# Optimization experiments

Hardware: AMD Instinct MI355X
Metric: run time of the kernel (lower is better)

## Reference

```python
import jax, jax.numpy as jnp
import numpy as np

B, T = 16, 40
NH, DEPTH, NCLASS, IMG_H, W_IMG = 128, 2, 6625, 32, 512
HIDDEN = 64  # nh < 256 -> hidden = 64
LINEAR_IN = NH * 8  # nh * int((32-3-1)/4+1)
BN_EPS = 1e-5


def _conv2d(x, w, b, stride, pad, groups=1):
    y = jax.lax.conv_general_dilated(
        x, w, (stride, stride), [(pad, pad), (pad, pad)],
        dimension_numbers=('NCHW', 'OIHW', 'NCHW'), feature_group_count=groups)
    return y + b[None, :, None, None]


def _conv_bn_act(x, w, b, g, bb, m, v, stride, pad, groups=1):
    y = _conv2d(x, w, b, stride, pad, groups)
    y = (y - m[None, :, None, None]) * jax.lax.rsqrt(v[None, :, None, None] + BN_EPS) \
        * g[None, :, None, None] + bb[None, :, None, None]
    return jax.nn.gelu(y, approximate=False)  # torch nn.GELU default = exact erf


def _gru(xs, wih, whh, bih, bhh):
    # torch GRU gate order: r, z, n. xs: [B, T, D] -> ys: [B, T, H]
    H = whh.shape[1]
    xp = jnp.einsum('btd,gd->btg', xs, wih) + bih  # [B,T,3H]

    def step(h, xt):
        hp = h @ whh.T + bhh
        r = jax.nn.sigmoid(xt[:, :H] + hp[:, :H])
        z = jax.nn.sigmoid(xt[:, H:2 * H] + hp[:, H:2 * H])
        n = jnp.tanh(xt[:, 2 * H:] + r * hp[:, 2 * H:])
        hn = (1.0 - z) * n + z * h
        return hn, hn

    h0 = jnp.zeros((xs.shape[0], H), xs.dtype)
    _, ys = jax.lax.scan(step, h0, jnp.swapaxes(xp, 0, 1))
    return jnp.swapaxes(ys, 0, 1)


def _forward(x, targets,
             conv0_w, conv0_b, bn0_g, bn0_b, bn0_m, bn0_v,
             blk_dw_w, blk_dw_b, blk_bn1_g, blk_bn1_b, blk_bn1_m, blk_bn1_v,
             blk_pw_w, blk_pw_b, blk_bn2_g, blk_bn2_b, blk_bn2_m, blk_bn2_v,
             enc_wih, enc_whh, enc_bih, enc_bhh,
             dec_wih, dec_whh, dec_bih, dec_bhh,
             emb, q_w, q_b, k_w, k_b, e_w, e_b, fc_w, fc_b):
    h = _conv_bn_act(x, conv0_w, conv0_b, bn0_g, bn0_b, bn0_m, bn0_v, 4, 0)  # [B,NH,8,128]
    # NOTE: original code applies each MicroBlock to the SAME x (feat = block(x)); faithful here.
    feat = h
    for i in range(DEPTH):
        t = h + _conv_bn_act(h, blk_dw_w[i], blk_dw_b[i], blk_bn1_g[i], blk_bn1_b[i],
                             blk_bn1_m[i], blk_bn1_v[i], 1, 1, groups=NH)
        feat = _conv_bn_act(t, blk_pw_w[i], blk_pw_b[i], blk_bn2_g[i], blk_bn2_b[i],
                            blk_bn2_m[i], blk_bn2_v[i], 1, 0)
    Bq, C, Hf, Wf = feat.shape
    feat_v = feat.reshape(Bq, C * Hf, Wf)  # Flatten(1,2)
    # adaptive_avg_pool1d target = W/4 == Wf -> identity
    feat_v = jnp.transpose(feat_v, (0, 2, 1))  # [B, Wf, C*Hf]
    enc = _gru(feat_v, enc_wih, enc_whh, enc_bih, enc_bhh)  # [B,Wf,H]
    out_enc = enc[:, -1:, :]  # [B,1,H]
    tgt = emb[targets]  # [B,T,H]
    in_dec = jnp.concatenate([out_enc, tgt], axis=1)  # [B,T+1,H]
    y = _gru(in_dec, dec_wih, dec_whh, dec_bih, dec_bhh)  # [B,T+1,H]
    q = y @ q_w.T + q_b  # [B,Td,NH]
    k = _conv2d(feat, k_w, k_b, 1, 1)  # [B,NH,h,w]
    t2 = jnp.tanh(k[:, None] + q[:, :, :, None, None])  # [B,Td,NH,h,w]
    e = jnp.einsum('btchw,c->bthw', t2, e_w[0]) + e_b[0]  # conv1x1_2: Linear(NH,1)
    a = jax.nn.softmax(e.reshape(Bq, e.shape[1], -1), axis=-1).reshape(e.shape)
    attn_feat = jnp.einsum('bchw,bthw->btc', feat, a)  # [B,Td,NH]
    # dropout: eval mode -> identity
    return attn_feat @ fc_w.T + fc_b  # [B,Td,NCLASS]


def setup_inputs() -> dict:
    key = jax.random.key(0)
    ks = iter(jax.random.split(key, 64))

    def rn(shape, s=0.05):
        return jax.random.normal(next(ks), shape, jnp.float32) * s

    inp = {
        'x': jax.random.normal(next(ks), (B, 3, IMG_H, W_IMG), jnp.float32),
        'targets': jax.random.randint(next(ks), (B, T), 0, NCLASS),
        'conv0_w': rn((NH, 3, 4, 4)), 'conv0_b': rn((NH,)),
        'bn0_g': jnp.ones((NH,)), 'bn0_b': jnp.zeros((NH,)),
        'bn0_m': jnp.zeros((NH,)), 'bn0_v': jnp.ones((NH,)),
        'blk_dw_w': rn((DEPTH, NH, 1, 3, 3)), 'blk_dw_b': rn((DEPTH, NH)),
        'blk_bn1_g': jnp.ones((DEPTH, NH)), 'blk_bn1_b': jnp.zeros((DEPTH, NH)),
        'blk_bn1_m': jnp.zeros((DEPTH, NH)), 'blk_bn1_v': jnp.ones((DEPTH, NH)),
        'blk_pw_w': rn((DEPTH, NH, NH, 1, 1)), 'blk_pw_b': rn((DEPTH, NH)),
        'blk_bn2_g': jnp.ones((DEPTH, NH)), 'blk_bn2_b': jnp.zeros((DEPTH, NH)),
        'blk_bn2_m': jnp.zeros((DEPTH, NH)), 'blk_bn2_v': jnp.ones((DEPTH, NH)),
        'enc_wih': rn((3 * HIDDEN, LINEAR_IN)), 'enc_whh': rn((3 * HIDDEN, HIDDEN)),
        'enc_bih': jnp.zeros((3 * HIDDEN,)), 'enc_bhh': jnp.zeros((3 * HIDDEN,)),
        'dec_wih': rn((3 * HIDDEN, HIDDEN)), 'dec_whh': rn((3 * HIDDEN, HIDDEN)),
        'dec_bih': jnp.zeros((3 * HIDDEN,)), 'dec_bhh': jnp.zeros((3 * HIDDEN,)),
        'emb': rn((NCLASS, HIDDEN)).at[1].set(0.0),  # padding_idx=1
        'q_w': rn((NH, HIDDEN)), 'q_b': jnp.zeros((NH,)),
        'k_w': rn((NH, NH, 3, 3)), 'k_b': jnp.zeros((NH,)),
        'e_w': rn((1, NH)), 'e_b': jnp.zeros((1,)),
        'fc_w': rn((NCLASS, NH)), 'fc_b': jnp.zeros((NCLASS,)),
    }
    return inp


def reference(x, targets,
              conv0_w, conv0_b, bn0_g, bn0_b, bn0_m, bn0_v,
              blk_dw_w, blk_dw_b, blk_bn1_g, blk_bn1_b, blk_bn1_m, blk_bn1_v,
              blk_pw_w, blk_pw_b, blk_bn2_g, blk_bn2_b, blk_bn2_m, blk_bn2_v,
              enc_wih, enc_whh, enc_bih, enc_bhh,
              dec_wih, dec_whh, dec_bih, dec_bhh,
              emb, q_w, q_b, k_w, k_b, e_w, e_b, fc_w, fc_b):
    return _forward(x, targets,
                    conv0_w, conv0_b, bn0_g, bn0_b, bn0_m, bn0_v,
                    blk_dw_w, blk_dw_b, blk_bn1_g, blk_bn1_b, blk_bn1_m, blk_bn1_v,
                    blk_pw_w, blk_pw_b, blk_bn2_g, blk_bn2_b, blk_bn2_m, blk_bn2_v,
                    enc_wih, enc_whh, enc_bih, enc_bhh,
                    dec_wih, dec_whh, dec_bih, dec_bhh,
                    emb, q_w, q_b, k_w, k_b, e_w, e_b, fc_w, fc_b)
```

## Files before the change

### kernel.cpp

```cpp
#include <hip/hip_runtime.h>
#include <hip/hip_bf16.h>

#define DEV __device__ __forceinline__

#define B_    16
#define T_    40
#define TDEC  41
#define NH    128
#define HF    8
#define WF    128
#define HID   64
#define G3    192
#define NCLS  6625
#define SPAT  1024
#define NFRAG 415

typedef _Float16 half8 __attribute__((ext_vector_type(8)));
typedef _Float16 half2_ __attribute__((ext_vector_type(2)));
typedef float    f32x4 __attribute__((ext_vector_type(4)));
typedef float    f32x2 __attribute__((ext_vector_type(2)));

#if __has_builtin(__builtin_amdgcn_fdot2)
#define FDOT2(w,h,acc) __builtin_amdgcn_fdot2((w),(h),(acc),false)
#else
#define FDOT2(w,h,acc) ((acc) + (float)((w)[0])*(float)((h)[0]) + (float)((w)[1])*(float)((h)[1]))
#endif

DEV float sigmoidf_(float x){ return 1.0f/(1.0f + __expf(-x)); }
DEV float tanhf_(float x){ float e = __expf(2.0f*x); return 1.0f - 2.0f/(e + 1.0f); }
DEV float gelu_(float x){ return 0.5f*x*(1.0f + erff(x*0.70710678118654752f)); }
DEV float bnf_(float x, float g, float b, float m, float v){
  return (x - m)*rsqrtf(v + 1e-5f)*g + b;
}

__global__ __launch_bounds__(256) void k_conv0(const float* __restrict__ x,
    const float* __restrict__ w, const float* __restrict__ bias,
    const float* __restrict__ bng, const float* __restrict__ bnb,
    const float* __restrict__ bnm, const float* __restrict__ bnv,
    float* __restrict__ h)
{
  int tid = blockIdx.x*256 + threadIdx.x;
  int ow = tid & 127;
  int oh = (tid >> 7) & 7;
  int c4 = (tid >> 10) & 31;
  int b  = tid >> 15;
  float acc[4] = {0.f,0.f,0.f,0.f};
  int xbase = ((b*3)*32 + oh*4)*512 + ow*4;
  for (int ci = 0; ci < 3; ++ci){
    #pragma unroll
    for (int kh = 0; kh < 4; ++kh){
      float4 xv = *(const float4*)(x + xbase + ci*(32*512) + kh*512);
      #pragma unroll
      for (int cc = 0; cc < 4; ++cc){
        int co = c4*4 + cc;
        const float* wp = w + ((co*3 + ci)*4 + kh)*4;
        acc[cc] += xv.x*wp[0] + xv.y*wp[1] + xv.z*wp[2] + xv.w*wp[3];
      }
    }
  }
  #pragma unroll
  for (int cc = 0; cc < 4; ++cc){
    int co = c4*4 + cc;
    float v = acc[cc] + bias[co];
    v = bnf_(v, bng[co], bnb[co], bnm[co], bnv[co]);
    h[((b*NH + co)*HF + oh)*WF + ow] = gelu_(v);
  }
}

__global__ __launch_bounds__(256) void k_dw(const float* __restrict__ h,
    const float* __restrict__ dww, const float* __restrict__ dwb,
    const float* __restrict__ g1, const float* __restrict__ b1,
    const float* __restrict__ m1, const float* __restrict__ v1,
    float* __restrict__ t)
{
  int tid = blockIdx.x*256 + threadIdx.x;
  int ow = tid & 127;
  int oh = (tid >> 7) & 7;
  int c  = (tid >> 10) & 127;
  int b  = tid >> 17;
  const float* wp = dww + NH*9 + c*9;
  const float* hp = h + ((b*NH + c)*HF)*WF;
  float acc = 0.f;
  #pragma unroll
  for (int kh = 0; kh < 3; ++kh){
    int ih = oh + kh - 1;
    if (ih < 0 || ih >= HF) continue;
    #pragma unroll
    for (int kw = 0; kw < 3; ++kw){
      int iw = ow + kw - 1;
      if (iw < 0 || iw >= WF) continue;
      acc += hp[ih*WF + iw]*wp[kh*3 + kw];
    }
  }
  float val = acc + dwb[NH + c];
  val = bnf_(val, g1[NH + c], b1[NH + c], m1[NH + c], v1[NH + c]);
  t[tid] = hp[oh*WF + ow] + gelu_(val);
}

__global__ __launch_bounds__(256) void k_fcprep(const float* __restrict__ fcw,
    _Float16* __restrict__ fcwH, _Float16* __restrict__ fcwL)
{
  int tid = blockIdx.x*256 + threadIdx.x;
  if (tid >= NFRAG*4*64*8) return;
  int j  = tid & 7;
  int l  = (tid >> 3) & 63;
  int kf = (tid >> 9) & 3;
  int nf = tid >> 11;
  int n = nf*16 + (l & 15);
  int k = kf*32 + ((l >> 4) << 3) + j;
  float v = (n < NCLS) ? fcw[n*NH + k] : 0.f;
  _Float16 hi = (_Float16)v;
  fcwH[tid] = hi;
  fcwL[tid] = (_Float16)(v - (float)hi);
}

__global__ __launch_bounds__(256) void k_misc(const float* __restrict__ pw,
    float* __restrict__ pwT, const float* __restrict__ kw,
    _Float16* __restrict__ kwA, const int* __restrict__ tgt,
    const float* __restrict__ emb, float* __restrict__ indec,
    const float* __restrict__ encwhh, unsigned* __restrict__ enc16,
    const float* __restrict__ decwhh, unsigned* __restrict__ dec16,
    const float* __restrict__ wih, _Float16* __restrict__ wihH,
    _Float16* __restrict__ wihL)
{
  int bid = blockIdx.x;
  if (bid < 64){
    int tid = bid*256 + threadIdx.x;
    int ci = tid & 127; int co = tid >> 7;
    pwT[ci*128 + co] = pw[16384 + co*128 + ci];
  } else if (bid < 640){
    int tid = (bid - 64)*256 + threadIdx.x;
    int j = tid & 7;
    int l = (tid >> 3) & 63;
    int f = (tid >> 9) & 7;
    int s = tid >> 12;
    int co = f*16 + (l & 15);
    int k  = s*32 + ((l >> 4) << 3) + j;
    int r  = k >> 7;
    int ci = k & 127;
    kwA[tid] = (_Float16)kw[(co*128 + ci)*9 + r];
  } else if (bid < 800){
    int tid = (bid - 640)*256 + threadIdx.x;
    if (tid >= B_*T_*HID) return;
    int j = tid & 63; int rest = tid >> 6;
    int t = rest % T_; int b = rest / T_;
    int cls = tgt[b*T_ + t];
    indec[(b*TDEC + 1 + t)*HID + j] = emb[cls*HID + j];
  } else if (bid < 848){
    int seg = bid - 800;
    const float* src = (seg < 24) ? encwhh : decwhh;
    unsigned* dst    = (seg < 24) ? enc16   : dec16;
    int tid = (seg % 24)*256 + threadIdx.x;
    int r = tid >> 5; int k2 = tid & 31;
    half2_ hv;
    hv[0] = (_Float16)src[r*HID + 2*k2];
    hv[1] = (_Float16)src[r*HID + 2*k2 + 1];
    dst[tid] = __builtin_bit_cast(unsigned, hv);
  } else {
    int tid = (bid - 848)*256 + threadIdx.x;
    if (tid >= 12*32*64*8) return;
    int j  = tid & 7;
    int l  = (tid >> 3) & 63;
    int kf = (tid >> 9) & 31;
    int nf = tid >> 14;
    int n = nf*16 + (l & 15);
    int k = kf*32 + ((l >> 4) << 3) + j;
    float v = wih[n*1024 + k];
    _Float16 hi = (_Float16)v;
    wihH[tid] = hi;
    wihL[tid] = (_Float16)(v - (float)hi);
  }
}

__global__ __launch_bounds__(512) void k_pw(const float* __restrict__ t,
    const float* __restrict__ pwT, const float* __restrict__ pwb,
    const float* __restrict__ g2, const float* __restrict__ b2,
    const float* __restrict__ m2, const float* __restrict__ v2,
    float* __restrict__ feat)
{
  int bid = blockIdx.x;
  int wh = bid & 1; int oh = (bid >> 1) & 7; int b = bid >> 4;
  int w0 = wh*64;
  int tid = threadIdx.x;
  __shared__ __align__(16) float tile[128*64];
  for (int i = 0; i < 16; ++i){
    int e = i*512 + tid; int ci = e >> 6; int wloc = e & 63;
    tile[ci*64 + wloc] = t[((b*NH + ci)*HF + oh)*WF + w0 + wloc];
  }
  __syncthreads();
  int co = tid & 127; int wq = tid >> 7;
  float acc[16];
  #pragma unroll
  for (int i = 0; i < 16; ++i) acc[i] = 0.f;
  for (int ci = 0; ci < 128; ++ci){
    float wt = pwT[ci*128 + co];
    const float4* tp = (const float4*)(tile + ci*64 + wq*16);
    #pragma unroll
    for (int j = 0; j < 4; ++j){
      float4 tv = tp[j];
      acc[j*4+0] += tv.x*wt; acc[j*4+1] += tv.y*wt;
      acc[j*4+2] += tv.z*wt; acc[j*4+3] += tv.w*wt;
    }
  }
  float bb = pwb[128 + co];
  float gg = g2[128 + co], bc = b2[128 + co], mm = m2[128 + co], vv = v2[128 + co];
  float* op = feat + ((b*NH + co)*HF + oh)*WF + w0 + wq*16;
  #pragma unroll
  for (int i = 0; i < 16; ++i){
    float v = bnf_(acc[i] + bb, gg, bc, mm, vv);
    op[i] = gelu_(v);
  }
}

__global__ __launch_bounds__(64) void k_encxp3(const float* __restrict__ feat,
    const uint4* __restrict__ wihH, const uint4* __restrict__ wihL,
    const float* __restrict__ bih, float* __restrict__ xp)
{
  int bid = blockIdx.x;
  int mf = bid & 127;
  int ny = bid >> 7;
  int l  = threadIdx.x;
  int b  = mf >> 3, wc = mf & 7;
  int m_w = wc*16 + (l & 15);
  f32x4 acc0{0.f,0.f,0.f,0.f}, acc1{0.f,0.f,0.f,0.f}, acc2{0.f,0.f,0.f,0.f};
  int nf0 = ny*3;
  for (int kf = 0; kf < 32; ++kf){
    int ci = kf*4 + (l >> 4);
    const float* ap = feat + ((b*NH + ci)*HF)*WF + m_w;
    float av[8];
    #pragma unroll
    for (int j = 0; j < 8; ++j) av[j] = ap[j*WF];
    half8 ah, al;
    #pragma unroll
    for (int j = 0; j < 8; ++j){
      ah[j] = (_Float16)av[j];
      al[j] = (_Float16)(av[j] - (float)ah[j]);
    }
    uint4 bH0 = wihH[((nf0+0)*32 + kf)*64 + l];
    uint4 bL0 = wihL[((nf0+0)*32 + kf)*64 + l];
    uint4 bH1 = wihH[((nf0+1)*32 + kf)*64 + l];
    uint4 bL1 = wihL[((nf0+1)*32 + kf)*64 + l];
    uint4 bH2 = wihH[((nf0+2)*32 + kf)*64 + l];
    uint4 bL2 = wihL[((nf0+2)*32 + kf)*64 + l];
    #define ACCUM(accv, bH, bL) {                                              \
      half8 wh = __builtin_bit_cast(half8, bH);                                \
      half8 wl = __builtin_bit_cast(half8, bL);                                \
      accv = __builtin_amdgcn_mfma_f32_16x16x32_f16(ah, wh, accv, 0, 0, 0);    \
      accv = __builtin_amdgcn_mfma_f32_16x16x32_f16(al, wh, accv, 0, 0, 0);    \
      accv = __builtin_amdgcn_mfma_f32_16x16x32_f16(ah, wl, accv, 0, 0, 0);    \
    }
    ACCUM(acc0, bH0, bL0)
    ACCUM(acc1, bH1, bL1)
    ACCUM(acc2, bH2, bL2)
    #undef ACCUM
  }
  int mbase = b*WF + wc*16 + ((l >> 4) << 2);
  #pragma unroll
  for (int i = 0; i < 3; ++i){
    f32x4 a = (i == 0) ? acc0 : (i == 1) ? acc1 : acc2;
    int n = (nf0 + i)*16 + (l & 15);
    float bias = bih[n];
    #pragma unroll
    for (int q = 0; q < 4; ++q)
      xp[(mbase + q)*G3 + n] = a[q] + bias;
  }
}

template<int STEPS, bool WRITE_ALL>
__global__ __attribute__((amdgpu_waves_per_eu(1, 1))) __launch_bounds__(64)
void k_scan2(const float* __restrict__ xp, const uint4* __restrict__ whh16,
             const float* __restrict__ bhh, float* __restrict__ outp)
{
  __shared__ __align__(16) _Float16 hsh16[HID];
  int g = threadIdx.x;
  int b = blockIdx.x;
  uint4 w0q[8], w1q[8], w2q[8];
  const uint4* q0 = whh16 + g*8;
  const uint4* q1 = whh16 + (HID + g)*8;
  const uint4* q2 = whh16 + (2*HID + g)*8;
  #pragma unroll
  for (int k = 0; k < 8; ++k){ w0q[k] = q0[k]; w1q[k] = q1[k]; w2q[k] = q2[k]; }
  float b0 = bhh[g], b1 = bhh[HID + g], b2 = bhh[2*HID + g];
  float hg = 0.f;
  hsh16[g] = (_Float16)0.f;
  const float* xpb = xp + b*STEPS*G3;
  float x0a = xpb[g], x1a = xpb[HID + g], x2a = xpb[2*HID + g];
  float x0b = 0.f, x1b = 0.f, x2b = 0.f;
  if (STEPS > 1){
    const float* p = xpb + G3 + g;
    x0b = p[0]; x1b = p[HID]; x2b = p[2*HID];
  }
  for (int t = 0; t < STEPS; ++t){
    float x0c = 0.f, x1c = 0.f, x2c = 0.f;
    if (t + 2 < STEPS){
      const float* p = xpb + (t + 2)*G3 + g;
      x0c = p[0]; x1c = p[HID]; x2c = p[2*HID];
    }
    const uint4* h4 = (const uint4*)hsh16;
    float a0 = b0, a1 = b1, a2 = b2;
    float d0 = 0.f, d1 = 0.f, d2 = 0.f;
    #pragma unroll
    for (int i = 0; i < 8; i += 2){
      uint4 hvA = h4[i], hvB = h4[i+1];
      #define DO4(hv, wq, aa, bb, cc)                                          \
      { half2_ h0 = __builtin_bit_cast(half2_, hv.x);                          \
        half2_ h1 = __builtin_bit_cast(half2_, hv.y);                          \
        half2_ h2 = __builtin_bit_cast(half2_, hv.z);                          \
        half2_ h3 = __builtin_bit_cast(half2_, hv.w);                          \
        aa = FDOT2(__builtin_bit_cast(half2_, w0q[wq].x), h0, aa);             \
        bb = FDOT2(__builtin_bit_cast(half2_, w1q[wq].x), h0, bb);             \
        cc = FDOT2(__builtin_bit_cast(half2_, w2q[wq].x), h0, cc);             \
        aa = FDOT2(__builtin_bit_cast(half2_, w0q[wq].y), h1, aa);             \
        bb = FDOT2(__builtin_bit_cast(half2_, w1q[wq].y), h1, bb);             \
        cc = FDOT2(__builtin_bit_cast(half2_, w2q[wq].y), h1, cc);             \
        aa = FDOT2(__builtin_bit_cast(half2_, w0q[wq].z), h2, aa);             \
        bb = FDOT2(__builtin_bit_cast(half2_, w1q[wq].z), h2, bb);             \
        cc = FDOT2(__builtin_bit_cast(half2_, w2q[wq].z), h2, cc);             \
        aa = FDOT2(__builtin_bit_cast(half2_, w0q[wq].w), h3, aa);             \
        bb = FDOT2(__builtin_bit_cast(half2_, w1q[wq].w), h3, bb);             \
        cc = FDOT2(__builtin_bit_cast(half2_, w2q[wq].w), h3, cc); }
      DO4(hvA, i,   a0, a1, a2)
      DO4(hvB, i+1, d0, d1, d2)
      #undef DO4
    }
    float hp0 = a0 + d0;
    float hp1 = a1 + d1;
    float hp2 = a2 + d2;
    float e0 = __expf(-(x0a + hp0));
    float r  = __builtin_amdgcn_rcpf(1.0f + e0);
    float e1 = __expf(-(x1a + hp1));
    float z  = __builtin_amdgcn_rcpf(1.0f + e1);
    float ag = x2a + r*hp2;
    float ex = __expf(2.0f*ag);
    float n  = 1.0f - 2.0f*__builtin_amdgcn_rcpf(ex + 1.0f);
    hg = z*(hg - n) + n;
    if (WRITE_ALL) outp[(b*TDEC + t)*HID + g] = hg;
    hsh16[g] = (_Float16)hg;
    x0a = x0b; x1a = x1b; x2a = x2b;
    x0b = x0c; x1b = x1c; x2b = x2c;
  }
  if (!WRITE_ALL) outp[(b*TDEC)*HID + g] = hg;
}

__global__ __launch_bounds__(64) void k_kconv3(const float* __restrict__ feat,
    const uint4* __restrict__ kwA4, const float* __restrict__ kb,
    float* __restrict__ ko)
{
  int bid = blockIdx.x;
  int b  = ((bid & 7) << 1) | ((bid >> 3) & 1);
  int mq = (bid >> 4) & 3;
  int cs = (bid >> 6) & 3;
  int wq = (bid >> 8) & 1;
  int oh = (bid >> 9) & 7;
  int l  = threadIdx.x;
  int w0 = wq*64 + mq*16;
  int iwb = w0 + (l & 15);
  int cib = (l >> 4) << 3;

  f32x4 acc0{0.f,0.f,0.f,0.f}, acc1{0.f,0.f,0.f,0.f};
  uint4 a0A, a0B, a1A, a1B;
  float b0v[8], b1v[8];

  #define ISS(s, aX, aY, bvv) {                                               \
    aX = kwA4[(s)*512 + cs*128 + l];                                          \
    aY = kwA4[(s)*512 + cs*128 + 64 + l];                                     \
    int r = (s) >> 2; int dh = r/3 - 1; int dw2 = r%3 - 1;                    \
    int ci0 = ((s) & 3) << 5;                                                 \
    int ih = oh + dh; int iw = iwb + dw2;                                     \
    bool ok = (ih >= 0) & (ih < HF) & (iw >= 0) & (iw < WF);                  \
    const float* fp = feat + ((b*NH + ci0 + cib)*HF + ih)*WF + iw;            \
    _Pragma("unroll")                                                         \
    for (int jj = 0; jj < 8; ++jj) bvv[jj] = ok ? fp[jj*(HF*WF)] : 0.f;       \
  }
  #define CMP(aX, aY, bvv) {                                                  \
    half8 bf;                                                                 \
    _Pragma("unroll")                                                         \
    for (int jj = 0; jj < 8; ++jj) bf[jj] = (_Float16)bvv[jj];                \
    half8 af0 = __builtin_bit_cast(half8, aX);                                \
    half8 af1 = __builtin_bit_cast(half8, aY);                                \
    acc0 = __builtin_amdgcn_mfma_f32_16x16x32_f16(af0, bf, acc0, 0, 0, 0);    \
    acc1 = __builtin_amdgcn_mfma_f32_16x16x32_f16(af1, bf, acc1, 0, 0, 0);    \
  }

  ISS(0, a0A, a0B, b0v);
  for (int s = 0; s < 36; s += 2){
    if (s + 1 < 36) ISS(s + 1, a1A, a1B, b1v);
    CMP(a0A, a0B, b0v);
    if (s + 2 < 36) ISS(s + 2, a0A, a0B, b0v);
    if (s + 1 < 36) CMP(a1A, a1B, b1v);
  }
  #undef ISS
  #undef CMP

  int m = w0 + (l & 15);
  #pragma unroll
  for (int q = 0; q < 4; ++q){
    int co0 = cs*32 + ((l >> 4) << 2) + q;
    int co1 = co0 + 16;
    ko[((b*NH + co0)*HF + oh)*WF + m] = acc0[q] + kb[co0];
    ko[((b*NH + co1)*HF + oh)*WF + m] = acc1[q] + kb[co1];
  }
}

__global__ void k_xpd(const float* __restrict__ indec, const float* __restrict__ wih,
                      const float* __restrict__ bih, float* __restrict__ xpd)
{
  int tid = blockIdx.x*256 + threadIdx.x;
  if (tid >= B_*TDEC*G3) return;
  int g = tid % G3; int bt = tid / G3;
  const float4* r4 = (const float4*)(indec + bt*HID);
  const float4* w4 = (const float4*)(wih + g*HID);
  float acc = bih[g];
  #pragma unroll
  for (int j = 0; j < 16; ++j){
    float4 rv = r4[j], wv = w4[j];
    acc += rv.x*wv.x + rv.y*wv.y + rv.z*wv.z + rv.w*wv.w;
  }
  xpd[tid] = acc;
}

__global__ void k_q(const float* __restrict__ y, const float* __restrict__ qw,
                    const float* __restrict__ qb0, float* __restrict__ q)
{
  int tid = blockIdx.x*256 + threadIdx.x;
  if (tid >= B_*TDEC*NH) return;
  int co = tid & 127; int bt = tid >> 7;
  const float4* r4 = (const float4*)(y + bt*HID);
  const float4* w4 = (const float4*)(qw + co*HID);
  float acc = qb0[co];
  #pragma unroll
  for (int j = 0; j < 16; ++j){
    float4 rv = r4[j], wv = w4[j];
    acc += rv.x*wv.x + rv.y*wv.y + rv.z*wv.z + rv.w*wv.w;
  }
  q[tid] = acc;
}

__global__ __launch_bounds__(512) void k_e3(const float* __restrict__ k,
    const float* __restrict__ q, const float* __restrict__ ew,
    const float* __restrict__ eb, float* __restrict__ e)
{
  int bid = blockIdx.x;
  int st = bid & 15; int b = bid >> 4;
  int s0 = st*64;
  int tid = threadIdx.x;
  __shared__ float ksh[NH*64];
  __shared__ float qsh[TDEC*NH];
  __shared__ float ewsh[NH];
  #pragma unroll
  for (int i = 0; i < 16; ++i){
    int e2 = i*512 + tid; int c = e2 >> 6; int j = e2 & 63;
    ksh[e2] = k[(b*NH + c)*SPAT + s0 + j];
  }
  #pragma unroll
  for (int i = 0; i < 11; ++i){
    int e2 = i*512 + tid;
    if (e2 < TDEC*NH) qsh[e2] = q[b*TDEC*NH + e2];
  }
  if (tid < NH) ewsh[tid] = ew[tid];
  __syncthreads();
  int sl = tid & 63; int tp = tid >> 6;
  float ebv = eb[0];
  float acc[6] = {ebv, ebv, ebv, ebv, ebv, ebv};
  #pragma unroll 2
  for (int c = 0; c < NH; ++c){
    float kv = ksh[c*64 + sl];
    float ewc = ewsh[c];
    #pragma unroll
    for (int i = 0; i < 6; ++i){
      int t = tp + i*8;
      if (t < TDEC){
        float v = kv + qsh[t*NH + c];
        float ex = __expf(2.0f*v);
        float rc = __builtin_amdgcn_rcpf(ex + 1.0f);
        acc[i] += ewc*(1.0f - 2.0f*rc);
      }
    }
  }
  #pragma unroll
  for (int i = 0; i < 6; ++i){
    int t = tp + i*8;
    if (t < TDEC) e[(b*TDEC + t)*SPAT + s0 + sl] = acc[i];
  }
}

__global__ __launch_bounds__(256) void k_attnf2(const float* __restrict__ feat,
    const float* __restrict__ e, float* __restrict__ attnf)
{
  int bid = blockIdx.x;
  int ch = bid & 1; int rest = bid >> 1;
  int tq = rest % 11; int b = rest / 11;
  int tid = threadIdx.x;
  __shared__ __align__(16) float ash[4*SPAT];
  __shared__ float psh[4*4*64];
  __shared__ float sinv[4];
  for (int i = 0; i < 16; ++i){
    int e2 = i*256 + tid; int tt = e2 >> 10; int s = e2 & 1023;
    int t = tq*4 + tt;
    ash[e2] = (t < TDEC) ? e[(b*TDEC + t)*SPAT + s] : 0.f;
  }
  __syncthreads();
  {
    int w = tid >> 6; int l = tid & 63;
    float* row = ash + w*SPAT;
    float vreg[16];
    float mx = -1e30f;
    #pragma unroll
    for (int j = 0; j < 16; ++j){ vreg[j] = row[l + j*64]; mx = fmaxf(mx, vreg[j]); }
    #pragma unroll
    for (int m = 1; m < 64; m <<= 1) mx = fmaxf(mx, __shfl_xor(mx, m));
    float sum = 0.f;
    #pragma unroll
    for (int j = 0; j < 16; ++j){
      float ev = __expf(vreg[j] - mx);
      row[l + j*64] = ev;
      sum += ev;
    }
    #pragma unroll
    for (int m = 1; m < 64; m <<= 1) sum += __shfl_xor(sum, m);
    if (l == 0) sinv[w] = 1.0f/sum;
  }
  __syncthreads();
  int cl = tid & 63; int sq = tid >> 6;
  const float* fp = feat + (b*NH + ch*64 + cl)*SPAT + sq*256;
  float acc[4] = {0.f,0.f,0.f,0.f};
  for (int i = 0; i < 64; ++i){
    float4 fv = *(const float4*)(fp + i*4);
    #pragma unroll
    for (int tt = 0; tt < 4; ++tt){
      const float* ar = ash + tt*SPAT + sq*256 + i*4;
      acc[tt] += fv.x*ar[0] + fv.y*ar[1] + fv.z*ar[2] + fv.w*ar[3];
    }
  }
  #pragma unroll
  for (int tt = 0; tt < 4; ++tt) psh[(sq*4 + tt)*64 + cl] = acc[tt];
  __syncthreads();
  {
    int tt = tid >> 6; int c2 = tid & 63;
    int t = tq*4 + tt;
    if (t < TDEC){
      float v = psh[(0*4 + tt)*64 + c2] + psh[(1*4 + tt)*64 + c2]
              + psh[(2*4 + tt)*64 + c2] + psh[(3*4 + tt)*64 + c2];
      attnf[(b*TDEC + t)*NH + ch*64 + c2] = v*sinv[tt];
    }
  }
}

__global__ __launch_bounds__(256) void k_fc2(const float* __restrict__ attnf,
    const uint4* __restrict__ fcwH, const uint4* __restrict__ fcwL,
    const float* __restrict__ fcb, float* __restrict__ out)
{
  int mf = blockIdx.x;
  int ny = blockIdx.y;
  int tid = threadIdx.x;
  int l = tid & 63, w = tid >> 6;
  half8 ah[4], al[4];
  const float* ap = attnf + (mf*16 + (l & 15))*NH + ((l >> 4) << 3);
  #pragma unroll
  for (int kf = 0; kf < 4; ++kf){
    float4 v0 = *(const float4*)(ap + kf*32);
    float4 v1 = *(const float4*)(ap + kf*32 + 4);
    float vv[8] = {v0.x, v0.y, v0.z, v0.w, v1.x, v1.y, v1.z, v1.w};
    half8 h, lo;
    #pragma unroll
    for (int j = 0; j < 8; ++j){
      h[j]  = (_Float16)vv[j];
      lo[j] = (_Float16)(vv[j] - (float)h[j]);
    }
    ah[kf] = h; al[kf] = lo;
  }
  #pragma unroll
  for (int i = 0; i < 4; ++i){
    int nf = ny*16 + w*4 + i;
    if (nf >= NFRAG) return;
    f32x4 acc{0.f,0.f,0.f,0.f};
    #pragma unroll
    for (int kf = 0; kf < 4; ++kf){
      uint4 bH = fcwH[(nf*4 + kf)*64 + l];
      uint4 bL = fcwL[(nf*4 + kf)*64 + l];
      half8 wh = __builtin_bit_cast(half8, bH);
      half8 wl = __builtin_bit_cast(half8, bL);
      acc = __builtin_amdgcn_mfma_f32_16x16x32_f16(ah[kf], wh, acc, 0, 0, 0);
      acc = __builtin_amdgcn_mfma_f32_16x16x32_f16(al[kf], wh, acc, 0, 0, 0);
      acc = __builtin_amdgcn_mfma_f32_16x16x32_f16(ah[kf], wl, acc, 0, 0, 0);
    }
    int n = nf*16 + (l & 15);
    if (n < NCLS){
      float bias = fcb[n];
      int mrow = mf*16 + ((l >> 4) << 2);
      #pragma unroll
      for (int q = 0; q < 4; ++q)
        out[(mrow + q)*NCLS + n] = acc[q] + bias;
    }
  }
}

extern "C" void kernel_launch(void* const* d_in, const int* in_sizes, int n_in,
                              void* d_out, int out_size, void* d_ws, size_t ws_size,
                              hipStream_t stream)
{
  (void)in_sizes; (void)n_in; (void)out_size; (void)ws_size;
  const float* x      = (const float*)d_in[0];
  const int*   tgt    = (const int*)  d_in[1];
  const float* conv0w = (const float*)d_in[2];
  const float* conv0b = (const float*)d_in[3];
  const float* bn0g   = (const float*)d_in[4];
  const float* bn0b   = (const float*)d_in[5];
  const float* bn0m   = (const float*)d_in[6];
  const float* bn0v   = (const float*)d_in[7];
  const float* dww    = (const float*)d_in[8];
  const float* dwb    = (const float*)d_in[9];
  const float* bn1g   = (const float*)d_in[10];
  const float* bn1b   = (const float*)d_in[11];
  const float* bn1m   = (const float*)d_in[12];
  const float* bn1v   = (const float*)d_in[13];
  const float* pww    = (const float*)d_in[14];
  const float* pwb    = (const float*)d_in[15];
  const float* bn2g   = (const float*)d_in[16];
  const float* bn2b   = (const float*)d_in[17];
  const float* bn2m   = (const float*)d_in[18];
  const float* bn2v   = (const float*)d_in[19];
  const float* encwih = (const float*)d_in[20];
  const float* encwhh = (const float*)d_in[21];
  const float* encbih = (const float*)d_in[22];
  const float* encbhh = (const float*)d_in[23];
  const float* decwih = (const float*)d_in[24];
  const float* decwhh = (const float*)d_in[25];
  const float* decbih = (const float*)d_in[26];
  const float* decbhh = (const float*)d_in[27];
  const float* emb    = (const float*)d_in[28];
  const float* qw     = (const float*)d_in[29];
  const float* qb0    = (const float*)d_in[30];
  const float* kw     = (const float*)d_in[31];
  const float* kb     = (const float*)d_in[32];
  const float* ew     = (const float*)d_in[33];
  const float* eb     = (const float*)d_in[34];
  const float* fcw    = (const float*)d_in[35];
  const float* fcb    = (const float*)d_in[36];

  float* ws    = (float*)d_ws;
  float* hbuf  = ws + 0;
  float* tbuf  = ws + 2097152;
  float* feat  = ws + 4194304;
  float* xp    = ws + 6291456;
  float* indec = ws + 6684672;
  float* xpd   = ws + 6726656;
  float* ybuf  = ws + 6852608;
  float* qbuf  = ws + 6894592;
  float* attf  = ws + 6978560;
  float* pwT   = ws + 7062528;
  _Float16* kwA = (_Float16*)(ws + 7078912);
  unsigned* enc16 = (unsigned*)(ws + 7152640);
  unsigned* dec16 = (unsigned*)(ws + 7158784);
  _Float16* fcwH = (_Float16*)(ws + 7164928);
  _Float16* fcwL = (_Float16*)(ws + 7589888);
  _Float16* wihH = (_Float16*)(ws + 6726656);
  _Float16* wihL = (_Float16*)(ws + 6852608);
  float* kbuf  = hbuf;
  float* ebuf  = tbuf;
  float* out   = (float*)d_out;

  hipLaunchKernelGGL(k_conv0,   dim3(2048),        dim3(256), 0, stream,
                     x, conv0w, conv0b, bn0g, bn0b, bn0m, bn0v, hbuf);
  hipLaunchKernelGGL(k_dw,      dim3(8192),        dim3(256), 0, stream,
                     hbuf, dww, dwb, bn1g, bn1b, bn1m, bn1v, tbuf);
  hipLaunchKernelGGL(k_misc,    dim3(1616),        dim3(256), 0, stream,
                     pww, pwT, kw, kwA, tgt, emb, indec,
                     encwhh, enc16, decwhh, dec16, encwih, wihH, wihL);
  hipLaunchKernelGGL(k_fcprep,  dim3(3320),        dim3(256), 0, stream,
                     fcw, fcwH, fcwL);
  hipLaunchKernelGGL(k_pw,      dim3(256),         dim3(512), 0, stream,
                     tbuf, pwT, pwb, bn2g, bn2b, bn2m, bn2v, feat);
  hipLaunchKernelGGL(k_encxp3,  dim3(512),         dim3(64), 0, stream,
                     feat, (const uint4*)wihH, (const uint4*)wihL, encbih, xp);
  hipLaunchKernelGGL((k_scan2<128,false>), dim3(16), dim3(64), 0, stream,
                     xp, (const uint4*)enc16, encbhh, indec);
  hipLaunchKernelGGL(k_kconv3,  dim3(4096),        dim3(64), 0, stream,
                     feat, (const uint4*)kwA, kb, kbuf);
  hipLaunchKernelGGL(k_xpd,     dim3(492),         dim3(256), 0, stream,
                     indec, decwih, decbih, xpd);
  hipLaunchKernelGGL((k_scan2<TDEC,true>), dim3(16), dim3(64), 0, stream,
                     xpd, (const uint4*)dec16, decbhh, ybuf);
  hipLaunchKernelGGL(k_q,       dim3(328),         dim3(256), 0, stream,
                     ybuf, qw, qb0, qbuf);
  hipLaunchKernelGGL(k_e3,      dim3(256),         dim3(512), 0, stream,
                     kbuf, qbuf, ew, eb, ebuf);
  hipLaunchKernelGGL(k_attnf2,  dim3(352),         dim3(256), 0, stream,
                     feat, ebuf, attf);
  hipLaunchKernelGGL(k_fc2,     dim3(41, 26),      dim3(256), 0, stream,
                     attf, (const uint4*)fcwH, (const uint4*)fcwL, fcb, out);
}
```

Measured before the change: 285.8 us.

## Fuse encoder GRU scan with key conv kernel to overlap execution

Merges the serial encoder GRU scan (16 blocks) and the independent 3x3 key convolution into one launch. The first 16 blocks run the scan at raised wave priority and the remaining 4096 blocks run the conv, so the latency-bound recurrence overlaps the conv instead of running alone. This removes a launch and a serialization point. The risk is that scan blocks may share CUs with conv blocks and run slower per step.

```diff
diff --git a/kernel.cpp b/kernel.cpp
--- a/kernel.cpp
+++ b/kernel.cpp
@@ -32,6 +32,57 @@
 DEV float bnf_(float x, float g, float b, float m, float v){
   return (x - m)*rsqrtf(v + 1e-5f)*g + b;
 }
+
+#define SCAN_LOOP(STEPS, WRITE_ALL)                                            \
+  for (int t = 0; t < (STEPS); ++t){                                           \
+    float x0c = 0.f, x1c = 0.f, x2c = 0.f;                                     \
+    if (t + 2 < (STEPS)){                                                      \
+      const float* p = xpb + (t + 2)*G3 + g;                                   \
+      x0c = p[0]; x1c = p[HID]; x2c = p[2*HID];                                \
+    }                                                                          \
+    const uint4* h4 = (const uint4*)hsh16;                                     \
+    float a0 = b0, a1 = b1, a2 = b2;                                           \
+    float d0 = 0.f, d1 = 0.f, d2 = 0.f;                                        \
+    _Pragma("unroll")                                                          \
+    for (int i = 0; i < 8; i += 2){                                            \
+      uint4 hvA = h4[i], hvB = h4[i+1];                                        \
+      DO4(hvA, i,   a0, a1, a2)                                                \
+      DO4(hvB, i+1, d0, d1, d2)                                                \
+    }                                                                          \
+    float hp0 = a0 + d0;                                                       \
+    float hp1 = a1 + d1;                                                       \
+    float hp2 = a2 + d2;                                                       \
+    float e0 = __expf(-(x0a + hp0));                                           \
+    float r  = __builtin_amdgcn_rcpf(1.0f + e0);                               \
+    float e1 = __expf(-(x1a + hp1));                                           \
+    float z  = __builtin_amdgcn_rcpf(1.0f + e1);                               \
+    float ag = x2a + r*hp2;                                                    \
+    float ex = __expf(2.0f*ag);                                                \
+    float n  = 1.0f - 2.0f*__builtin_amdgcn_rcpf(ex + 1.0f);                   \
+    hg = z*(hg - n) + n;                                                       \
+    if (WRITE_ALL) outp[(b*TDEC + t)*HID + g] = hg;                            \
+    hsh16[g] = (_Float16)hg;                                                   \
+    x0a = x0b; x1a = x1b; x2a = x2b;                                           \
+    x0b = x0c; x1b = x1c; x2b = x2c;                                           \
+  }
+
+#define DO4(hv, wq, aa, bb, cc)                                                \
+  { half2_ h0 = __builtin_bit_cast(half2_, hv.x);                              \
+    half2_ h1 = __builtin_bit_cast(half2_, hv.y);                              \
+    half2_ h2 = __builtin_bit_cast(half2_, hv.z);                              \
+    half2_ h3 = __builtin_bit_cast(half2_, hv.w);                              \
+    aa = FDOT2(__builtin_bit_cast(half2_, w0q[wq].x), h0, aa);                 \
+    bb = FDOT2(__builtin_bit_cast(half2_, w1q[wq].x), h0, bb);                 \
+    cc = FDOT2(__builtin_bit_cast(half2_, w2q[wq].x), h0, cc);                 \
+    aa = FDOT2(__builtin_bit_cast(half2_, w0q[wq].y), h1, aa);                 \
+    bb = FDOT2(__builtin_bit_cast(half2_, w1q[wq].y), h1, bb);                 \
+    cc = FDOT2(__builtin_bit_cast(half2_, w2q[wq].y), h1, cc);                 \
+    aa = FDOT2(__builtin_bit_cast(half2_, w0q[wq].z), h2, aa);                 \
+    bb = FDOT2(__builtin_bit_cast(half2_, w1q[wq].z), h2, bb);                 \
+    cc = FDOT2(__builtin_bit_cast(half2_, w2q[wq].z), h2, cc);                 \
+    aa = FDOT2(__builtin_bit_cast(half2_, w0q[wq].w), h3, aa);                 \
+    bb = FDOT2(__builtin_bit_cast(half2_, w1q[wq].w), h3, bb);                 \
+    cc = FDOT2(__builtin_bit_cast(half2_, w2q[wq].w), h3, cc); }
 
 __global__ __launch_bounds__(256) void k_conv0(const float* __restrict__ x,
     const float* __restrict__ w, const float* __restrict__ bias,
@@ -290,63 +341,44 @@
     const float* p = xpb + G3 + g;
     x0b = p[0]; x1b = p[HID]; x2b = p[2*HID];
   }
-  for (int t = 0; t < STEPS; ++t){
-    float x0c = 0.f, x1c = 0.f, x2c = 0.f;
-    if (t + 2 < STEPS){
-      const float* p = xpb + (t + 2)*G3 + g;
-      x0c = p[0]; x1c = p[HID]; x2c = p[2*HID];
-    }
-    const uint4* h4 = (const uint4*)hsh16;
-    float a0 = b0, a1 = b1, a2 = b2;
-    float d0 = 0.f, d1 = 0.f, d2 = 0.f;
-    #pragma unroll
-    for (int i = 0; i < 8; i += 2){
-      uint4 hvA = h4[i], hvB = h4[i+1];
-      #define DO4(hv, wq, aa, bb, cc)                                          \
-      { half2_ h0 = __builtin_bit_cast(half2_, hv.x);                          \
-        half2_ h1 = __builtin_bit_cast(half2_, hv.y);                          \
-        half2_ h2 = __builtin_bit_cast(half2_, hv.z);                          \
-        half2_ h3 = __builtin_bit_cast(half2_, hv.w);                          \
-        aa = FDOT2(__builtin_bit_cast(half2_, w0q[wq].x), h0, aa);             \
-        bb = FDOT2(__builtin_bit_cast(half2_, w1q[wq].x), h0, bb);             \
-        cc = FDOT2(__builtin_bit_cast(half2_, w2q[wq].x), h0, cc);             \
-        aa = FDOT2(__builtin_bit_cast(half2_, w0q[wq].y), h1, aa);             \
-        bb = FDOT2(__builtin_bit_cast(half2_, w1q[wq].y), h1, bb);             \
-        cc = FDOT2(__builtin_bit_cast(half2_, w2q[wq].y), h1, cc);             \
-        aa = FDOT2(__builtin_bit_cast(half2_, w0q[wq].z), h2, aa);             \
-        bb = FDOT2(__builtin_bit_cast(half2_, w1q[wq].z), h2, bb);             \
-        cc = FDOT2(__builtin_bit_cast(half2_, w2q[wq].z), h2, cc);             \
-        aa = FDOT2(__builtin_bit_cast(half2_, w0q[wq].w), h3, aa);             \
-        bb = FDOT2(__builtin_bit_cast(half2_, w1q[wq].w), h3, bb);             \
-        cc = FDOT2(__builtin_bit_cast(half2_, w2q[wq].w), h3, cc); }
-      DO4(hvA, i,   a0, a1, a2)
-      DO4(hvB, i+1, d0, d1, d2)
-      #undef DO4
-    }
-    float hp0 = a0 + d0;
-    float hp1 = a1 + d1;
-    float hp2 = a2 + d2;
-    float e0 = __expf(-(x0a + hp0));
-    float r  = __builtin_amdgcn_rcpf(1.0f + e0);
-    float e1 = __expf(-(x1a + hp1));
-    float z  = __builtin_amdgcn_rcpf(1.0f + e1);
-    float ag = x2a + r*hp2;
-    float ex = __expf(2.0f*ag);
-    float n  = 1.0f - 2.0f*__builtin_amdgcn_rcpf(ex + 1.0f);
-    hg = z*(hg - n) + n;
-    if (WRITE_ALL) outp[(b*TDEC + t)*HID + g] = hg;
-    hsh16[g] = (_Float16)hg;
-    x0a = x0b; x1a = x1b; x2a = x2b;
-    x0b = x0c; x1b = x1c; x2b = x2c;
-  }
+  SCAN_LOOP(STEPS, WRITE_ALL)
   if (!WRITE_ALL) outp[(b*TDEC)*HID + g] = hg;
 }
 
-__global__ __launch_bounds__(64) void k_kconv3(const float* __restrict__ feat,
-    const uint4* __restrict__ kwA4, const float* __restrict__ kb,
-    float* __restrict__ ko)
-{
-  int bid = blockIdx.x;
+__global__ __launch_bounds__(64) void k_escan_conv(
+    const float* __restrict__ xp, const uint4* __restrict__ whh16,
+    const float* __restrict__ bhh, float* __restrict__ outp,
+    const float* __restrict__ feat, const uint4* __restrict__ kwA4,
+    const float* __restrict__ kb, float* __restrict__ ko)
+{
+  __shared__ __align__(16) _Float16 hsh16[HID];
+  int bigid = blockIdx.x;
+  if (bigid < 16){
+    __builtin_amdgcn_s_setprio(3);
+    int g = threadIdx.x;
+    int b = bigid;
+    uint4 w0q[8], w1q[8], w2q[8];
+    const uint4* q0 = whh16 + g*8;
+    const uint4* q1 = whh16 + (HID + g)*8;
+    const uint4* q2 = whh16 + (2*HID + g)*8;
+    #pragma unroll
+    for (int k = 0; k < 8; ++k){ w0q[k] = q0[k]; w1q[k] = q1[k]; w2q[k] = q2[k]; }
+    float b0 = bhh[g], b1 = bhh[HID + g], b2 = bhh[2*HID + g];
+    float hg = 0.f;
+    hsh16[g] = (_Float16)0.f;
+    const float* xpb = xp + b*WF*G3;
+    float x0a = xpb[g], x1a = xpb[HID + g], x2a = xpb[2*HID + g];
+    float x0b = 0.f, x1b = 0.f, x2b = 0.f;
+    {
+      const float* p = xpb + G3 + g;
+      x0b = p[0]; x1b = p[HID]; x2b = p[2*HID];
+    }
+    SCAN_LOOP(WF, false)
+    outp[(b*TDEC)*HID + g] = hg;
+    __builtin_amdgcn_s_setprio(0);
+    return;
+  }
+  int bid = bigid - 16;
   int b  = ((bid & 7) << 1) | ((bid >> 3) & 1);
   int mq = (bid >> 4) & 3;
   int cs = (bid >> 6) & 3;
@@ -673,9 +705,8 @@
                      tbuf, pwT, pwb, bn2g, bn2b, bn2m, bn2v, feat);
   hipLaunchKernelGGL(k_encxp3,  dim3(512),         dim3(64), 0, stream,
                      feat, (const uint4*)wihH, (const uint4*)wihL, encbih, xp);
-  hipLaunchKernelGGL((k_scan2<128,false>), dim3(16), dim3(64), 0, stream,
-                     xp, (const uint4*)enc16, encbhh, indec);
-  hipLaunchKernelGGL(k_kconv3,  dim3(4096),        dim3(64), 0, stream,
+  hipLaunchKernelGGL(k_escan_conv, dim3(4112),     dim3(64), 0, stream,
+                     xp, (const uint4*)enc16, encbhh, indec,
                      feat, (const uint4*)kwA, kb, kbuf);
   hipLaunchKernelGGL(k_xpd,     dim3(492),         dim3(256), 0, stream,
                      indec, decwih, decbih, xpd);
```

Result: faster. 260.3 us (-8.9%).
